# Kernel optimization log

Hardware: AMD Instinct MI355X
Metric: run time of the kernel (lower is better)

Reference implementation:

```python
import jax, jax.numpy as jnp
import numpy as np

B, T, H, W, D, NH, DEPTH, NCODES = 2, 16, 16, 16, 512, 8, 6, 1024
HW = H * W; DH = D // NH; KH = KW = 3; SIZE = KH * KW; MLP_DIM = 2 * D
NEG = -1e9


def _ln(x, g, b, eps=1e-5):
    m = jnp.mean(x, -1, keepdims=True)
    v = jnp.mean((x - m) ** 2, -1, keepdims=True)
    return (x - m) * jax.lax.rsqrt(v + eps) * g + b


def _rope(x, pos):
    # x: [N, h, T, dh]; half-split rotary embedding
    half = x.shape[-1] // 2
    freqs = 1.0 / (10000.0 ** (jnp.arange(half, dtype=jnp.float32) / half))
    ang = pos[:, None] * freqs[None]            # [T, half]
    cos = jnp.concatenate([jnp.cos(ang), jnp.cos(ang)], -1)
    sin = jnp.concatenate([jnp.sin(ang), jnp.sin(ang)], -1)
    rot = jnp.concatenate([-x[..., half:], x[..., :half]], -1)
    return x * cos + rot * sin


def setup_inputs() -> dict:
    key = jax.random.key(0)
    keys = iter(jax.random.split(key, 64))
    def p(shape, s=0.02):
        return (s * jax.random.normal(next(keys), shape)).astype(jnp.float32)
    inp = dict(
        codes=jax.random.randint(next(keys), (B, T, HW), 0, NCODES),
        emb_table=p((NCODES, D)),
        cls_token=p((1, 1, 1, D)),
        h_emb=p((1, 1, H, D)),
        w_emb=p((1, 1, W, D)),
        emb_norm_g=jnp.ones(D), emb_norm_b=jnp.zeros(D),
        sn_g=jnp.ones((DEPTH, D)), sn_b=jnp.zeros((DEPTH, D)),
        s_wq=p((DEPTH, D, D)), s_bq=jnp.zeros((DEPTH, D)),
        s_wk=p((DEPTH, D, D)), s_bk=jnp.zeros((DEPTH, D)),
        s_wv=p((DEPTH, D, D)), s_bv=jnp.zeros((DEPTH, D)),
        s_wo=p((DEPTH, D, D)), s_bo=jnp.zeros((DEPTH, D)),
        tn_g=jnp.ones((DEPTH, D)), tn_b=jnp.zeros((DEPTH, D)),
        t_wq=p((DEPTH, D, D)), t_bq=jnp.zeros((DEPTH, D)),
        t_wk=p((DEPTH, D, D)), t_bk=jnp.zeros((DEPTH, D)),
        t_wv=p((DEPTH, D, D)), t_bv=jnp.zeros((DEPTH, D)),
        t_wo=p((DEPTH, D, D)), t_bo=jnp.zeros((DEPTH, D)),
        mn_g=jnp.ones((DEPTH, D)), mn_b=jnp.zeros((DEPTH, D)),
        mlp_w1=p((DEPTH, D, MLP_DIM)), mlp_b1=jnp.zeros((DEPTH, MLP_DIM)),
        mlp_w2=p((DEPTH, MLP_DIM, D)), mlp_b2=jnp.zeros((DEPTH, D)),
        fn_g=jnp.ones(D), fn_b=jnp.zeros(D),
    )
    return inp


def reference(codes, emb_table, cls_token, h_emb, w_emb, emb_norm_g, emb_norm_b,
              sn_g, sn_b, s_wq, s_bq, s_wk, s_bk, s_wv, s_bv, s_wo, s_bo,
              tn_g, tn_b, t_wq, t_bq, t_wk, t_bk, t_wv, t_bv, t_wo, t_bo,
              mn_g, mn_b, mlp_w1, mlp_b1, mlp_w2, mlp_b2, fn_g, fn_b):
    T1 = T + 1
    emb = emb_table[codes]                                   # [B,T,HW,D]
    # positional embeddings exactly as torch repeat / repeat_interleave
    x = emb + jnp.tile(h_emb, (1, 1, W, 1)) + jnp.repeat(w_emb, H, axis=2)
    x = jnp.concatenate([x, jnp.broadcast_to(cls_token, (B, 1, HW, D))], axis=1)
    x = _ln(x, emb_norm_g, emb_norm_b)                       # [B,T1,HW,D]

    # temporal causal mask: True = masked
    tmask = jnp.triu(jnp.ones((T1, T1), dtype=bool), 1).at[-1, -1].set(True)
    # spatial out-of-bounds mask [H,W,SIZE] from unfold of ones with zero pad
    ones_pad = jnp.pad(jnp.ones((H, W), jnp.float32), 1)
    smask = jnp.stack([ones_pad[a:a + H, b:b + W]
                       for a in range(KH) for b in range(KW)], -1) == 0

    scale = 1.0 / jnp.sqrt(jnp.float32(DH))
    pos = jnp.arange(T1, dtype=jnp.float32)
    k_list, v_list = [], []
    attn_logits = None
    for i in range(DEPTH):
        # ---- spatial windowed attention on frames 0..T-1 ----
        xg = x[:, :-1].reshape(B, T, H, W, D)
        xn = _ln(xg, sn_g[i], sn_b[i])
        pad = jnp.pad(xn, ((0, 0), (0, 0), (1, 1), (1, 1), (0, 0)))
        nb = jnp.stack([pad[:, :, a:a + H, b:b + W]
                        for a in range(KH) for b in range(KW)], axis=4)  # [B,T,H,W,SIZE,D]
        q = (xn @ s_wq[i] + s_bq[i]).reshape(B, T, H, W, NH, DH)
        kk = (nb @ s_wk[i] + s_bk[i]).reshape(B, T, H, W, SIZE, NH, DH)
        vv = (nb @ s_wv[i] + s_bv[i]).reshape(B, T, H, W, SIZE, NH, DH)
        lg = jnp.einsum('btxynd,btxysnd->btxyns', q, kk) * scale
        lg = jnp.where(smask[None, None, :, :, None, :], NEG, lg)
        a_sp = jax.nn.softmax(lg, -1)
        o = jnp.einsum('btxyns,btxysnd->btxynd', a_sp, vv).reshape(B, T, H, W, D)
        o = o @ s_wo[i] + s_bo[i]
        x_sp = (o + xg).reshape(B, T, HW, D)                 # residual (drop_path=id, eval)
        xt = jnp.concatenate([x_sp, x[:, -1:]], axis=1)      # [B,T1,HW,D]

        # ---- temporal RoPE causal attention over T1 per spatial location ----
        s = xt.transpose(0, 2, 1, 3).reshape(B * HW, T1, D)
        sn_ = _ln(s, tn_g[i], tn_b[i])
        def heads(y):
            return y.reshape(B * HW, T1, NH, DH).transpose(0, 2, 1, 3)
        qt = _rope(heads(sn_ @ t_wq[i] + t_bq[i]), pos)
        kt = _rope(heads(sn_ @ t_wk[i] + t_bk[i]), pos)
        vt = heads(sn_ @ t_wv[i] + t_bv[i])
        lt = jnp.einsum('nhqd,nhkd->nhqk', qt, kt) * scale
        lt = jnp.where(tmask[None, None], NEG, lt)
        at = jax.nn.softmax(lt, -1)
        ot = jnp.einsum('nhqk,nhkd->nhqd', at, vt).transpose(0, 2, 1, 3).reshape(B * HW, T1, D)
        s = (ot @ t_wo[i] + t_bo[i]) + s
        xo = s.reshape(B, HW, T1, D).transpose(0, 2, 1, 3)   # [B,T1,HW,D]
        # average frame 0 over HW and broadcast back (as in torch code)
        xo = xo.at[:, 0].set(jnp.broadcast_to(xo[:, 0].mean(axis=1, keepdims=True), (B, HW, D)))
        attn_logits = lt.reshape(B, HW, NH, T1, T1)

        # ---- MLP (dim -> 2*dim, tanh, -> dim), dropout off in eval ----
        y = jnp.tanh(_ln(xo, mn_g[i], mn_b[i]) @ mlp_w1[i] + mlp_b1[i]) @ mlp_w2[i] + mlp_b2[i]
        x = y + xo
        k_list.append(kt[:, :, :-1, :])
        v_list.append(vt[:, :, :-1, :])

    return _ln(x, fn_g, fn_b), attn_logits, jnp.stack(k_list), jnp.stack(v_list)
```

## Files before the change

kernel.cpp:

```cpp
#include <hip/hip_runtime.h>
#include <hip/hip_bf16.h>
#include <math.h>

#define D_    512
#define NHH   8
#define DH_   64
#define T_    16
#define T1_   17
#define HWL   256
#define B__   2
#define NEGV  -1e9f

typedef __attribute__((ext_vector_type(8))) short short8;
typedef __attribute__((ext_vector_type(4))) short short4v;
typedef __attribute__((ext_vector_type(4))) float f32x4;
typedef __hip_bfloat16 bf16;

__device__ inline float wave_sum(float v){
  #pragma unroll
  for(int o=32;o>0;o>>=1) v += __shfl_xor(v,o,64);
  return v;
}
__device__ inline float b2f(unsigned short s){
  unsigned u = ((unsigned)s)<<16; float f; __builtin_memcpy(&f,&u,4); return f;
}
__device__ inline short f2bs(float f){
  bf16 h = __float2bfloat16(f); short s; __builtin_memcpy(&s,&h,2); return s;
}
__device__ inline void gload_lds16(const void* g, void* l){
  __builtin_amdgcn_global_load_lds((const __attribute__((address_space(1))) void*)g,
                                   (__attribute__((address_space(3))) void*)l, 16, 0, 0);
}

__global__ __launch_bounds__(256) void embed_ln_kernel(
    const int* __restrict__ codes, const float* __restrict__ emb,
    const float* __restrict__ cls, const float* __restrict__ hpos,
    const float* __restrict__ wpos, const float* __restrict__ g,
    const float* __restrict__ bta, float* __restrict__ X){
  int row  = blockIdx.x*4 + (threadIdx.x>>6);
  int lane = threadIdx.x & 63;
  int hw = row % HWL; int bt = row / HWL; int t = bt % T1_; int bb = bt / T1_;
  float v[8];
  if(t < T_){
    int code = codes[(bb*T_ + t)*HWL + hw];
    const float* ep = emb  + (size_t)code*D_;
    const float* hp = hpos + (size_t)(hw & 15)*D_;
    const float* wp = wpos + (size_t)(hw >> 4)*D_;
    #pragma unroll
    for(int j=0;j<8;j++){ int d = lane + j*64; v[j] = ep[d] + hp[d] + wp[d]; }
  } else {
    #pragma unroll
    for(int j=0;j<8;j++) v[j] = cls[lane + j*64];
  }
  float s=0;
  #pragma unroll
  for(int j=0;j<8;j++) s += v[j];
  s = wave_sum(s);
  float mean = s*(1.f/512.f);
  float s2=0;
  #pragma unroll
  for(int j=0;j<8;j++){ float d0=v[j]-mean; s2 += d0*d0; }
  s2 = wave_sum(s2);
  float inv = rsqrtf(s2*(1.f/512.f) + 1e-5f);
  float* o = X + (size_t)row*D_;
  #pragma unroll
  for(int j=0;j<8;j++){ int d = lane + j*64; o[d] = (v[j]-mean)*inv*g[d] + bta[d]; }
}

__global__ __launch_bounds__(256) void ln_kernel(
    const float* __restrict__ in, float* __restrict__ out,
    const float* __restrict__ g, const float* __restrict__ bta,
    int c_rpb, int s_rpb){
  int row  = blockIdx.x*4 + (threadIdx.x>>6);
  int lane = threadIdx.x & 63;
  int bb = row / c_rpb; int rem = row - bb*c_rpb;
  const float4* p = (const float4*)(in + ((size_t)bb*s_rpb + rem)*D_);
  float4 a = p[lane], c = p[lane+64];
  float s = a.x+a.y+a.z+a.w + c.x+c.y+c.z+c.w;
  s = wave_sum(s);
  float mean = s*(1.f/512.f);
  float s2 = (a.x-mean)*(a.x-mean)+(a.y-mean)*(a.y-mean)+(a.z-mean)*(a.z-mean)+(a.w-mean)*(a.w-mean)
           + (c.x-mean)*(c.x-mean)+(c.y-mean)*(c.y-mean)+(c.z-mean)*(c.z-mean)+(c.w-mean)*(c.w-mean);
  s2 = wave_sum(s2);
  float inv = rsqrtf(s2*(1.f/512.f) + 1e-5f);
  const float4* g4 = (const float4*)g; const float4* b4 = (const float4*)bta;
  float4 gv=g4[lane], gw=g4[lane+64], bv=b4[lane], bw=b4[lane+64];
  float4 o0 = { (a.x-mean)*inv*gv.x+bv.x, (a.y-mean)*inv*gv.y+bv.y,
                (a.z-mean)*inv*gv.z+bv.z, (a.w-mean)*inv*gv.w+bv.w };
  float4 o1 = { (c.x-mean)*inv*gw.x+bw.x, (c.y-mean)*inv*gw.y+bw.y,
                (c.z-mean)*inv*gw.z+bw.z, (c.w-mean)*inv*gw.w+bw.w };
  float4* o = (float4*)(out + (size_t)row*D_);
  o[lane] = o0; o[lane+64] = o1;
}

__global__ __launch_bounds__(256) void ln_bf_kernel(
    const float* __restrict__ in, bf16* __restrict__ out,
    const float* __restrict__ g, const float* __restrict__ bta,
    int c_rpb, int s_rpb){
  int row  = blockIdx.x*4 + (threadIdx.x>>6);
  int lane = threadIdx.x & 63;
  int bb = row / c_rpb; int rem = row - bb*c_rpb;
  const float4* p = (const float4*)(in + ((size_t)bb*s_rpb + rem)*D_);
  float4 a = p[lane], c = p[lane+64];
  float s = a.x+a.y+a.z+a.w + c.x+c.y+c.z+c.w;
  s = wave_sum(s);
  float mean = s*(1.f/512.f);
  float s2 = (a.x-mean)*(a.x-mean)+(a.y-mean)*(a.y-mean)+(a.z-mean)*(a.z-mean)+(a.w-mean)*(a.w-mean)
           + (c.x-mean)*(c.x-mean)+(c.y-mean)*(c.y-mean)+(c.z-mean)*(c.z-mean)+(c.w-mean)*(c.w-mean);
  s2 = wave_sum(s2);
  float inv = rsqrtf(s2*(1.f/512.f) + 1e-5f);
  const float4* g4 = (const float4*)g; const float4* b4 = (const float4*)bta;
  float4 gv=g4[lane], gw=g4[lane+64], bv=b4[lane], bw=b4[lane+64];
  short4v r0 = { f2bs((a.x-mean)*inv*gv.x+bv.x), f2bs((a.y-mean)*inv*gv.y+bv.y),
                 f2bs((a.z-mean)*inv*gv.z+bv.z), f2bs((a.w-mean)*inv*gv.w+bv.w) };
  short4v r1 = { f2bs((c.x-mean)*inv*gw.x+bw.x), f2bs((c.y-mean)*inv*gw.y+bw.y),
                 f2bs((c.z-mean)*inv*gw.z+bw.z), f2bs((c.w-mean)*inv*gw.w+bw.w) };
  bf16* o = out + (size_t)row*D_;
  *(short4v*)&o[lane*4]       = r0;
  *(short4v*)&o[256 + lane*4] = r1;
}

__global__ __launch_bounds__(256) void wconv_kernel(
    const float* sq, const float* sk, const float* sv, const float* so,
    const float* tq, const float* tk, const float* tv, const float* to,
    const float* w1, const float* w2, bf16* __restrict__ dst){
  __shared__ float sm[32][33];
  int z = blockIdx.z; int i = z/10, id = z - i*10;
  const size_t wo = (size_t)i*262144, mo = (size_t)i*524288;
  bf16* db = dst + (size_t)i*3145728;
  const float* src; bf16* d; int K, N;
  switch(id){
    case 0: src=sq+wo; d=db+0*262144;  K=512;  N=512;  break;
    case 1: src=sk+wo; d=db+1*262144;  K=512;  N=512;  break;
    case 2: src=sv+wo; d=db+2*262144;  K=512;  N=512;  break;
    case 3: src=so+wo; d=db+3*262144;  K=512;  N=512;  break;
    case 4: src=tq+wo; d=db+4*262144;  K=512;  N=512;  break;
    case 5: src=tk+wo; d=db+5*262144;  K=512;  N=512;  break;
    case 6: src=tv+wo; d=db+6*262144;  K=512;  N=512;  break;
    case 7: src=to+wo; d=db+7*262144;  K=512;  N=512;  break;
    case 8: src=w1+mo; d=db+2097152;   K=512;  N=1024; break;
    default:src=w2+mo; d=db+2621440;   K=1024; N=512;  break;
  }
  int n0 = blockIdx.x<<5, k0 = blockIdx.y<<5;
  if(n0 >= N || k0 >= K) return;
  int tx = threadIdx.x & 31, ty = threadIdx.x >> 5;
  #pragma unroll
  for(int j=0;j<4;j++) sm[ty+j*8][tx] = src[(size_t)(k0+ty+j*8)*N + n0+tx];
  __syncthreads();
  #pragma unroll
  for(int j=0;j<4;j++) d[(size_t)(n0+ty+j*8)*K + k0+tx] = __float2bfloat16(sm[tx][ty+j*8]);
}

template<int ACT, bool RES, bool OBF>
__global__ __launch_bounds__(256) void gemm_mfma(
    const bf16* __restrict__ A, const bf16* __restrict__ Wt,
    const float* __restrict__ bias, void* __restrict__ outp,
    const float* __restrict__ resid, int K, int N, int c_rpb, int o_rpb){
  __shared__ __align__(16) bf16 As[128*64];
  __shared__ __align__(16) bf16 Bs[128*64];
  const int tid  = threadIdx.x;
  const int lane = tid & 63;
  const int w    = tid >> 6;
  const int row0 = blockIdx.y << 7;
  const int col0 = blockIdx.x << 7;
  const int mb = (w>>1)*64, nb = (w&1)*64;
  size_t ga[4], gb[4];
  #pragma unroll
  for(int r=0;r<4;r++){
    int c = (r*4+w)*64 + lane;
    int rw = c>>3;
    int ks = (c&7) ^ (rw&7);
    ga[r] = (size_t)(row0+rw)*K + (ks<<3);
    gb[r] = (size_t)(col0+rw)*K + (ks<<3);
  }
  f32x4 acc[4][4] = {};
  for(int k0=0;k0<K;k0+=64){
    #pragma unroll
    for(int r=0;r<4;r++){
      gload_lds16(A  + ga[r] + k0, As + (size_t)(r*4+w)*512);
      gload_lds16(Wt + gb[r] + k0, Bs + (size_t)(r*4+w)*512);
    }
    __syncthreads();
    const short8* Av = (const short8*)As;
    const short8* Bv = (const short8*)Bs;
    #pragma unroll
    for(int kk=0;kk<2;kk++){
      const int slot = (lane>>4) + kk*4;
      short8 af[4], bfr[4];
      #pragma unroll
      for(int mi=0;mi<4;mi++){ int rw = mb + mi*16 + (lane&15); af[mi]  = Av[rw*8 + (slot ^ (rw&7))]; }
      #pragma unroll
      for(int ni=0;ni<4;ni++){ int rw = nb + ni*16 + (lane&15); bfr[ni] = Bv[rw*8 + (slot ^ (rw&7))]; }
      #pragma unroll
      for(int mi=0;mi<4;mi++)
        #pragma unroll
        for(int ni=0;ni<4;ni++)
          acc[mi][ni] = __builtin_amdgcn_mfma_f32_16x16x32_bf16(af[mi], bfr[ni], acc[mi][ni], 0,0,0);
    }
    __syncthreads();
  }
  #pragma unroll
  for(int mi=0;mi<4;mi++){
    #pragma unroll
    for(int r=0;r<4;r++){
      int row = row0 + mb + mi*16 + (lane>>4)*4 + r;
      int bb = row / c_rpb;
      size_t orow = (size_t)bb*o_rpb + (row - bb*c_rpb);
      #pragma unroll
      for(int ni=0;ni<4;ni++){
        int col = col0 + nb + ni*16 + (lane&15);
        float v = acc[mi][ni][r] + bias[col];
        if(ACT==1) v = tanhf(v);
        if(RES) v += resid[orow*(size_t)N + col];
        if(OBF) ((bf16*)outp)[orow*(size_t)N + col] = __float2bfloat16(v);
        else    ((float*)outp)[orow*(size_t)N + col] = v;
      }
    }
  }
}

template<int ACT, bool RES, bool OBF>
__global__ __launch_bounds__(256) void gemm_mfma64(
    const bf16* __restrict__ A, const bf16* __restrict__ Wt,
    const float* __restrict__ bias, void* __restrict__ outp,
    const float* __restrict__ resid, int K, int N, int c_rpb, int o_rpb){
  __shared__ __align__(16) bf16 As[64*64];
  __shared__ __align__(16) bf16 Bs[64*64];
  const int tid  = threadIdx.x;
  const int lane = tid & 63;
  const int w    = tid >> 6;
  const int row0 = blockIdx.y << 6;
  const int col0 = blockIdx.x << 6;
  const int mw = (w>>1)*32, nw = (w&1)*32;
  size_t ga[2], gb[2];
  #pragma unroll
  for(int r=0;r<2;r++){
    int c = (r*4+w)*64 + lane;
    int rw = c>>3;
    int ks = (c&7) ^ (rw&7);
    ga[r] = (size_t)(row0+rw)*K + (ks<<3);
    gb[r] = (size_t)(col0+rw)*K + (ks<<3);
  }
  f32x4 acc[2][2] = {};
  for(int k0=0;k0<K;k0+=64){
    #pragma unroll
    for(int r=0;r<2;r++){
      gload_lds16(A  + ga[r] + k0, As + (size_t)(r*4+w)*512);
      gload_lds16(Wt + gb[r] + k0, Bs + (size_t)(r*4+w)*512);
    }
    __syncthreads();
    const short8* Av = (const short8*)As;
    const short8* Bv = (const short8*)Bs;
    #pragma unroll
    for(int kk=0;kk<2;kk++){
      const int slot = (lane>>4) + kk*4;
      short8 af[2], bfr[2];
      #pragma unroll
      for(int mi=0;mi<2;mi++){ int rw = mw + mi*16 + (lane&15); af[mi]  = Av[rw*8 + (slot ^ (rw&7))]; }
      #pragma unroll
      for(int ni=0;ni<2;ni++){ int rw = nw + ni*16 + (lane&15); bfr[ni] = Bv[rw*8 + (slot ^ (rw&7))]; }
      #pragma unroll
      for(int mi=0;mi<2;mi++)
        #pragma unroll
        for(int ni=0;ni<2;ni++)
          acc[mi][ni] = __builtin_amdgcn_mfma_f32_16x16x32_bf16(af[mi], bfr[ni], acc[mi][ni], 0,0,0);
    }
    __syncthreads();
  }
  #pragma unroll
  for(int mi=0;mi<2;mi++){
    #pragma unroll
    for(int r=0;r<4;r++){
      int row = row0 + mw + mi*16 + (lane>>4)*4 + r;
      int bb = row / c_rpb;
      size_t orow = (size_t)bb*o_rpb + (row - bb*c_rpb);
      #pragma unroll
      for(int ni=0;ni<2;ni++){
        int col = col0 + nw + ni*16 + (lane&15);
        float v = acc[mi][ni][r] + bias[col];
        if(ACT==1) v = tanhf(v);
        if(RES) v += resid[orow*(size_t)N + col];
        if(OBF) ((bf16*)outp)[orow*(size_t)N + col] = __float2bfloat16(v);
        else    ((float*)outp)[orow*(size_t)N + col] = v;
      }
    }
  }
}

__global__ __launch_bounds__(256) void gemm_qkv(
    const bf16* __restrict__ A, const bf16* __restrict__ Wt,
    const float* __restrict__ bq, const float* __restrict__ bk, const float* __restrict__ bv,
    bf16* __restrict__ Qo, bf16* __restrict__ Ko, bf16* __restrict__ Vo){
  const int K = 512;
  __shared__ __align__(16) bf16 As[128*64];
  __shared__ __align__(16) bf16 Bs[128*64];
  const int tid  = threadIdx.x;
  const int lane = tid & 63;
  const int w    = tid >> 6;
  const int row0 = blockIdx.y << 7;
  const int col0 = blockIdx.x << 7;
  const int mb = (w>>1)*64, nb = (w&1)*64;
  size_t ga[4], gb[4];
  #pragma unroll
  for(int r=0;r<4;r++){
    int c = (r*4+w)*64 + lane;
    int rw = c>>3;
    int ks = (c&7) ^ (rw&7);
    ga[r] = (size_t)(row0+rw)*K + (ks<<3);
    gb[r] = (size_t)(col0+rw)*K + (ks<<3);
  }
  f32x4 acc[4][4] = {};
  for(int k0=0;k0<K;k0+=64){
    #pragma unroll
    for(int r=0;r<4;r++){
      gload_lds16(A  + ga[r] + k0, As + (size_t)(r*4+w)*512);
      gload_lds16(Wt + gb[r] + k0, Bs + (size_t)(r*4+w)*512);
    }
    __syncthreads();
    const short8* Av = (const short8*)As;
    const short8* Bv = (const short8*)Bs;
    #pragma unroll
    for(int kk=0;kk<2;kk++){
      const int slot = (lane>>4) + kk*4;
      short8 af[4], bfr[4];
      #pragma unroll
      for(int mi=0;mi<4;mi++){ int rw = mb + mi*16 + (lane&15); af[mi]  = Av[rw*8 + (slot ^ (rw&7))]; }
      #pragma unroll
      for(int ni=0;ni<4;ni++){ int rw = nb + ni*16 + (lane&15); bfr[ni] = Bv[rw*8 + (slot ^ (rw&7))]; }
      #pragma unroll
      for(int mi=0;mi<4;mi++)
        #pragma unroll
        for(int ni=0;ni<4;ni++)
          acc[mi][ni] = __builtin_amdgcn_mfma_f32_16x16x32_bf16(af[mi], bfr[ni], acc[mi][ni], 0,0,0);
    }
    __syncthreads();
  }
  const int sel = col0 >> 9;
  bf16* outp = (sel==0) ? Qo : (sel==1 ? Ko : Vo);
  const float* bp = (sel==0) ? bq : (sel==1 ? bk : bv);
  const int cb = col0 & 511;
  #pragma unroll
  for(int mi=0;mi<4;mi++){
    #pragma unroll
    for(int r=0;r<4;r++){
      int row = row0 + mb + mi*16 + (lane>>4)*4 + r;
      #pragma unroll
      for(int ni=0;ni<4;ni++){
        int col = cb + nb + ni*16 + (lane&15);
        outp[(size_t)row*512 + col] = __float2bfloat16(acc[mi][ni][r] + bp[col]);
      }
    }
  }
}

__global__ __launch_bounds__(256) void spatial_attn_kernel(
    const bf16* __restrict__ Q, const bf16* __restrict__ K,
    const bf16* __restrict__ V, bf16* __restrict__ O){
  int loc = blockIdx.x;
  int hw = loc & 255;
  int hh = hw >> 4, ww = hw & 15;
  int tid = threadIdx.x, lane = tid & 63, w = tid >> 6;
  int h = w*2 + (lane>>5);
  int j = lane & 31;
  size_t base = (size_t)loc*D_ + h*DH_ + 2*j;
  unsigned uq = *(const unsigned*)&Q[base];
  float q0 = b2f((unsigned short)uq), q1 = b2f((unsigned short)(uq>>16));
  float lg[9]; int nrow[9];
  #pragma unroll
  for(int s=0;s<9;s++){
    int a = s/3 - 1, b2_ = s%3 - 1;
    int nh = hh + a, nw = ww + b2_;
    bool ok = ((unsigned)nh < 16u) && ((unsigned)nw < 16u);
    nrow[s] = ok ? (loc - hw + (nh<<4) + nw) : -1;
    float p = 0.f;
    if(ok){
      unsigned uk = *(const unsigned*)&K[(size_t)nrow[s]*D_ + h*DH_ + 2*j];
      p = q0*b2f((unsigned short)uk) + q1*b2f((unsigned short)(uk>>16));
    }
    #pragma unroll
    for(int o=16;o>0;o>>=1) p += __shfl_xor(p, o, 64);
    lg[s] = ok ? p*0.125f : NEGV;
  }
  float m = lg[0];
  #pragma unroll
  for(int s=1;s<9;s++) m = fmaxf(m, lg[s]);
  float den = 0.f, wv[9];
  #pragma unroll
  for(int s=0;s<9;s++){ wv[s] = __expf(lg[s]-m); den += wv[s]; }
  float inv = 1.f/den;
  float a0 = 0.f, a1 = 0.f;
  #pragma unroll
  for(int s=0;s<9;s++){
    if(nrow[s] >= 0){
      unsigned uv = *(const unsigned*)&V[(size_t)nrow[s]*D_ + h*DH_ + 2*j];
      a0 += wv[s]*b2f((unsigned short)uv);
      a1 += wv[s]*b2f((unsigned short)(uv>>16));
    }
  }
  unsigned up = (unsigned)(unsigned short)f2bs(a0*inv) | ((unsigned)(unsigned short)f2bs(a1*inv) << 16);
  *(unsigned*)&O[base] = up;
}

__global__ __launch_bounds__(512) void fused_tattn(
    const bf16* __restrict__ Qb, const bf16* __restrict__ Kb, const bf16* __restrict__ Vb,
    bf16* __restrict__ O, float* __restrict__ kout, float* __restrict__ vout,
    float* __restrict__ ltout, int write_lt){
  __shared__ __align__(16) bf16 Qs[17*520];
  __shared__ __align__(16) bf16 Ks[17*520];
  __shared__ __align__(16) bf16 Vs[17*512];
  __shared__ float Ws[8][17][18];
  const int tid = threadIdx.x, w = tid>>6, lane = tid&63;
  const int hw = blockIdx.x & 255, b = blockIdx.x >> 8;
  const size_t tstr = (size_t)HWL*D_;
  const size_t rb0 = ((size_t)(b*T1_)*HWL + hw)*D_;
  for(int t=w; t<17; t+=8){
    size_t src = rb0 + (size_t)t*tstr + lane*8;
    *(short8*)&Qs[t*520 + lane*8] = *(const short8*)&Qb[src];
    *(short8*)&Ks[t*520 + lane*8] = *(const short8*)&Kb[src];
    *(short8*)&Vs[t*512 + lane*8] = *(const short8*)&Vb[src];
  }
  __syncthreads();
  {
    int i = lane & 31;
    float freq = __expf(-9.210340372f * (float)i * (1.f/32.f));
    bf16* P = (lane < 32) ? Qs : Ks;
    #pragma unroll
    for(int t=0;t<17;t++){
      float sn, cs; __sincosf((float)t*freq, &sn, &cs);
      int idx = t*520 + w*64 + i;
      float x1 = __bfloat162float(P[idx]);
      float x2 = __bfloat162float(P[idx+32]);
      P[idx]    = __float2bfloat16(x1*cs - x2*sn);
      P[idx+32] = __float2bfloat16(x2*cs + x1*sn);
    }
  }
  __syncthreads();
  {
    size_t eb = (((size_t)(b*HWL + hw)*NHH + w)*16)*64 + lane;
    #pragma unroll
    for(int t=0;t<16;t++){
      kout[eb + t*64] = __bfloat162float(Ks[t*520 + w*64 + lane]);
      vout[eb + t*64] = __bfloat162float(Vs[t*512 + w*64 + lane]);
    }
  }
  size_t lb = ((size_t)(b*HWL + hw)*NHH + w)*289;
  for(int p=lane; p<289; p+=64){
    int t = p/17, u = p - t*17;
    float d = 0.f;
    #pragma unroll
    for(int jj=0;jj<8;jj++){
      short8 qq = *(short8*)&Qs[t*520 + w*64 + jj*8];
      short8 kk = *(short8*)&Ks[u*520 + w*64 + jj*8];
      #pragma unroll
      for(int e=0;e<8;e++) d += b2f((unsigned short)qq[e]) * b2f((unsigned short)kk[e]);
    }
    bool masked = (u > t) || (t == 16 && u == 16);
    float lg = masked ? NEGV : d*0.125f;
    Ws[w][t][u] = lg;
    if(write_lt) ltout[lb + t*17 + u] = lg;
  }
  __syncthreads();
  if(lane < 17){
    float m = -1e30f;
    #pragma unroll
    for(int u=0;u<17;u++) m = fmaxf(m, Ws[w][lane][u]);
    float den = 0.f, e[17];
    #pragma unroll
    for(int u=0;u<17;u++){ e[u] = __expf(Ws[w][lane][u]-m); den += e[u]; }
    float inv = 1.f/den;
    #pragma unroll
    for(int u=0;u<17;u++) Ws[w][lane][u] = e[u]*inv;
  }
  __syncthreads();
  float Vr[17];
  #pragma unroll
  for(int u=0;u<17;u++) Vr[u] = __bfloat162float(Vs[u*512 + w*64 + lane]);
  #pragma unroll
  for(int t=0;t<17;t++){
    float acc = 0.f;
    #pragma unroll
    for(int u=0;u<17;u++) acc += Ws[w][t][u]*Vr[u];
    O[rb0 + (size_t)t*tstr + w*64 + lane] = __float2bfloat16(acc);
  }
}

__global__ __launch_bounds__(256) void avg_frame0_kernel(float* __restrict__ X){
  int d = blockIdx.x & 511; int bb = blockIdx.x >> 9;
  int hw = threadIdx.x;
  __shared__ float sm[256];
  size_t idx = ((size_t)(bb*T1_)*HWL + hw)*D_ + d;
  sm[hw] = X[idx];
  __syncthreads();
  for(int o=128;o>0;o>>=1){ if(hw<o) sm[hw] += sm[hw+o]; __syncthreads(); }
  X[idx] = sm[0]*(1.f/256.f);
}

extern "C" void kernel_launch(void* const* d_in, const int* in_sizes, int n_in,
                              void* d_out, int out_size, void* d_ws, size_t ws_size,
                              hipStream_t stream){
  const int*   codes = (const int*)  d_in[0];
  const float* emb   = (const float*)d_in[1];
  const float* cls   = (const float*)d_in[2];
  const float* hpos  = (const float*)d_in[3];
  const float* wpos  = (const float*)d_in[4];
  const float* eng   = (const float*)d_in[5];
  const float* enb   = (const float*)d_in[6];
  const float* sn_g  = (const float*)d_in[7];
  const float* sn_b  = (const float*)d_in[8];
  const float* s_wq  = (const float*)d_in[9];
  const float* s_bq  = (const float*)d_in[10];
  const float* s_wk  = (const float*)d_in[11];
  const float* s_bk  = (const float*)d_in[12];
  const float* s_wv  = (const float*)d_in[13];
  const float* s_bv  = (const float*)d_in[14];
  const float* s_wo  = (const float*)d_in[15];
  const float* s_bo  = (const float*)d_in[16];
  const float* tn_g  = (const float*)d_in[17];
  const float* tn_b  = (const float*)d_in[18];
  const float* t_wq  = (const float*)d_in[19];
  const float* t_bq  = (const float*)d_in[20];
  const float* t_wk  = (const float*)d_in[21];
  const float* t_bk  = (const float*)d_in[22];
  const float* t_wv  = (const float*)d_in[23];
  const float* t_bv  = (const float*)d_in[24];
  const float* t_wo  = (const float*)d_in[25];
  const float* t_bo  = (const float*)d_in[26];
  const float* mn_g  = (const float*)d_in[27];
  const float* mn_b  = (const float*)d_in[28];
  const float* mw1   = (const float*)d_in[29];
  const float* mb1   = (const float*)d_in[30];
  const float* mw2   = (const float*)d_in[31];
  const float* mb2   = (const float*)d_in[32];
  const float* fn_g  = (const float*)d_in[33];
  const float* fn_b  = (const float*)d_in[34];

  float* ws = (float*)d_ws;
  const size_t NX = 4456448;
  float* X   = ws;
  bf16*  XNb = (bf16*)(X + NX);
  bf16*  Qb  = (bf16*)((float*)XNb + NX/2);
  bf16*  Kb  = (bf16*)((float*)Qb  + NX/2);
  bf16*  Vb  = (bf16*)((float*)Kb  + NX/2);
  bf16*  Wt  = (bf16*)((float*)Vb  + NX/2);
  bf16*  HIDb= Qb;

  float* out0 = (float*)d_out;
  float* out1 = out0 + NX;
  float* out2 = out1 + 1183744;
  float* out3 = out2 + 25165824;

  const int RS = B__*T_*HWL;
  const int RT = B__*T1_*HWL;
  dim3 gQs(12, 64);
  dim3 gQt(12, 68);
  dim3 g64s(8, 128);
  dim3 g64t(8, 136);
  dim3 gM1(8, 68);
  dim3 wcg(32, 32, 60);

  embed_ln_kernel<<<RT/4, 256, 0, stream>>>(codes, emb, cls, hpos, wpos, eng, enb, X);
  wconv_kernel<<<wcg,256,0,stream>>>(s_wq, s_wk, s_wv, s_wo, t_wq, t_wk, t_wv, t_wo, mw1, mw2, Wt);

  for(int i=0;i<6;i++){
    bf16* Wl = Wt + (size_t)i*3145728;
    ln_bf_kernel<<<RS/4,256,0,stream>>>(X, XNb, sn_g+i*D_, sn_b+i*D_, T_*HWL, T1_*HWL);
    gemm_qkv<<<gQs,256,0,stream>>>(XNb, Wl, s_bq+i*D_, s_bk+i*D_, s_bv+i*D_, Qb, Kb, Vb);
    spatial_attn_kernel<<<RS,256,0,stream>>>(Qb, Kb, Vb, XNb);
    gemm_mfma64<0,true,false><<<g64s,256,0,stream>>>(XNb, Wl+3*262144, s_bo+i*D_, X, X, 512, 512, T_*HWL, T1_*HWL);
    ln_bf_kernel<<<RT/4,256,0,stream>>>(X, XNb, tn_g+i*D_, tn_b+i*D_, T1_*HWL, T1_*HWL);
    gemm_qkv<<<gQt,256,0,stream>>>(XNb, Wl+4*262144, t_bq+i*D_, t_bk+i*D_, t_bv+i*D_, Qb, Kb, Vb);
    fused_tattn<<<512,512,0,stream>>>(Qb, Kb, Vb, XNb,
                                      out2+(size_t)i*4194304, out3+(size_t)i*4194304,
                                      out1, (i==5)?1:0);
    gemm_mfma64<0,true,false><<<g64t,256,0,stream>>>(XNb, Wl+7*262144, t_bo+i*D_, X, X, 512, 512, RT, RT);
    avg_frame0_kernel<<<1024,256,0,stream>>>(X);
    ln_bf_kernel<<<RT/4,256,0,stream>>>(X, XNb, mn_g+i*D_, mn_b+i*D_, T1_*HWL, T1_*HWL);
    gemm_mfma<1,false,true ><<<gM1,256,0,stream>>>(XNb, Wl+2097152, mb1+i*1024, HIDb, nullptr, 512, 1024, RT, RT);
    gemm_mfma64<0,true,false><<<g64t,256,0,stream>>>(HIDb, Wl+2621440, mb2+i*D_, X, X, 1024, 512, RT, RT);
  }
  ln_kernel<<<RT/4,256,0,stream>>>(X, out0, fn_g, fn_b, T1_*HWL, T1_*HWL);
}
```

Measured before the change: 1.362 ms.

## Store residual stream in bf16 and double-buffer the 64-tile GEMM

Switches the residual activation buffer X from fp32 to bf16 across embedding, all layer norms, residual GEMM epilogues, frame-0 averaging and the final norm. The aim is to halve the memory traffic spent reading and writing the residual stream. It also adds LDS double buffering to gemm_mfma64, so the next K-tile loads while the current one is computed, and vectorises the embedding loads. The cost is accumulated rounding error in the residual over six layers, which could hurt accuracy against the fp32 reference.

New measurement: 1.363 ms. No clear change (+0.1%).

```diff
diff --git a/kernel.cpp b/kernel.cpp
--- a/kernel.cpp
+++ b/kernel.cpp
@@ -36,21 +36,25 @@
     const int* __restrict__ codes, const float* __restrict__ emb,
     const float* __restrict__ cls, const float* __restrict__ hpos,
     const float* __restrict__ wpos, const float* __restrict__ g,
-    const float* __restrict__ bta, float* __restrict__ X){
+    const float* __restrict__ bta, bf16* __restrict__ X){
   int row  = blockIdx.x*4 + (threadIdx.x>>6);
   int lane = threadIdx.x & 63;
   int hw = row % HWL; int bt = row / HWL; int t = bt % T1_; int bb = bt / T1_;
   float v[8];
   if(t < T_){
     int code = codes[(bb*T_ + t)*HWL + hw];
-    const float* ep = emb  + (size_t)code*D_;
-    const float* hp = hpos + (size_t)(hw & 15)*D_;
-    const float* wp = wpos + (size_t)(hw >> 4)*D_;
-    #pragma unroll
-    for(int j=0;j<8;j++){ int d = lane + j*64; v[j] = ep[d] + hp[d] + wp[d]; }
+    const float4* ep = (const float4*)(emb  + (size_t)code*D_);
+    const float4* hp = (const float4*)(hpos + (size_t)(hw & 15)*D_);
+    const float4* wp = (const float4*)(wpos + (size_t)(hw >> 4)*D_);
+    float4 a0=ep[lane*2], a1=ep[lane*2+1];
+    float4 h0=hp[lane*2], h1=hp[lane*2+1];
+    float4 w0=wp[lane*2], w1=wp[lane*2+1];
+    v[0]=a0.x+h0.x+w0.x; v[1]=a0.y+h0.y+w0.y; v[2]=a0.z+h0.z+w0.z; v[3]=a0.w+h0.w+w0.w;
+    v[4]=a1.x+h1.x+w1.x; v[5]=a1.y+h1.y+w1.y; v[6]=a1.z+h1.z+w1.z; v[7]=a1.w+h1.w+w1.w;
   } else {
-    #pragma unroll
-    for(int j=0;j<8;j++) v[j] = cls[lane + j*64];
+    const float4* cp = (const float4*)cls;
+    float4 c0=cp[lane*2], c1=cp[lane*2+1];
+    v[0]=c0.x; v[1]=c0.y; v[2]=c0.z; v[3]=c0.w; v[4]=c1.x; v[5]=c1.y; v[6]=c1.z; v[7]=c1.w;
   }
   float s=0;
   #pragma unroll
@@ -62,62 +66,73 @@
   for(int j=0;j<8;j++){ float d0=v[j]-mean; s2 += d0*d0; }
   s2 = wave_sum(s2);
   float inv = rsqrtf(s2*(1.f/512.f) + 1e-5f);
-  float* o = X + (size_t)row*D_;
-  #pragma unroll
-  for(int j=0;j<8;j++){ int d = lane + j*64; o[d] = (v[j]-mean)*inv*g[d] + bta[d]; }
+  const float4* g4 = (const float4*)g; const float4* b4 = (const float4*)bta;
+  float4 gv=g4[lane*2], gw=g4[lane*2+1], bv=b4[lane*2], bw=b4[lane*2+1];
+  short4v r0 = { f2bs((v[0]-mean)*inv*gv.x+bv.x), f2bs((v[1]-mean)*inv*gv.y+bv.y),
+                 f2bs((v[2]-mean)*inv*gv.z+bv.z), f2bs((v[3]-mean)*inv*gv.w+bv.w) };
+  short4v r1 = { f2bs((v[4]-mean)*inv*gw.x+bw.x), f2bs((v[5]-mean)*inv*gw.y+bw.y),
+                 f2bs((v[6]-mean)*inv*gw.z+bw.z), f2bs((v[7]-mean)*inv*gw.w+bw.w) };
+  bf16* o = X + (size_t)row*D_;
+  *(short4v*)&o[lane*8]     = r0;
+  *(short4v*)&o[lane*8 + 4] = r1;
 }
 
 __global__ __launch_bounds__(256) void ln_kernel(
-    const float* __restrict__ in, float* __restrict__ out,
+    const bf16* __restrict__ in, float* __restrict__ out,
     const float* __restrict__ g, const float* __restrict__ bta,
     int c_rpb, int s_rpb){
   int row  = blockIdx.x*4 + (threadIdx.x>>6);
   int lane = threadIdx.x & 63;
   int bb = row / c_rpb; int rem = row - bb*c_rpb;
-  const float4* p = (const float4*)(in + ((size_t)bb*s_rpb + rem)*D_);
-  float4 a = p[lane], c = p[lane+64];
-  float s = a.x+a.y+a.z+a.w + c.x+c.y+c.z+c.w;
+  short8 vv = *(const short8*)(in + ((size_t)bb*s_rpb + rem)*D_ + lane*8);
+  float v[8]; float s=0;
+  #pragma unroll
+  for(int j=0;j<8;j++){ v[j] = b2f((unsigned short)vv[j]); s += v[j]; }
   s = wave_sum(s);
   float mean = s*(1.f/512.f);
-  float s2 = (a.x-mean)*(a.x-mean)+(a.y-mean)*(a.y-mean)+(a.z-mean)*(a.z-mean)+(a.w-mean)*(a.w-mean)
-           + (c.x-mean)*(c.x-mean)+(c.y-mean)*(c.y-mean)+(c.z-mean)*(c.z-mean)+(c.w-mean)*(c.w-mean);
+  float s2=0;
+  #pragma unroll
+  for(int j=0;j<8;j++){ float d0=v[j]-mean; s2 += d0*d0; }
   s2 = wave_sum(s2);
   float inv = rsqrtf(s2*(1.f/512.f) + 1e-5f);
   const float4* g4 = (const float4*)g; const float4* b4 = (const float4*)bta;
-  float4 gv=g4[lane], gw=g4[lane+64], bv=b4[lane], bw=b4[lane+64];
-  float4 o0 = { (a.x-mean)*inv*gv.x+bv.x, (a.y-mean)*inv*gv.y+bv.y,
-                (a.z-mean)*inv*gv.z+bv.z, (a.w-mean)*inv*gv.w+bv.w };
-  float4 o1 = { (c.x-mean)*inv*gw.x+bw.x, (c.y-mean)*inv*gw.y+bw.y,
-                (c.z-mean)*inv*gw.z+bw.z, (c.w-mean)*inv*gw.w+bw.w };
-  float4* o = (float4*)(out + (size_t)row*D_);
-  o[lane] = o0; o[lane+64] = o1;
+  float4 gv=g4[lane*2], gw=g4[lane*2+1], bv=b4[lane*2], bw=b4[lane*2+1];
+  float4 o0 = { (v[0]-mean)*inv*gv.x+bv.x, (v[1]-mean)*inv*gv.y+bv.y,
+                (v[2]-mean)*inv*gv.z+bv.z, (v[3]-mean)*inv*gv.w+bv.w };
+  float4 o1 = { (v[4]-mean)*inv*gw.x+bw.x, (v[5]-mean)*inv*gw.y+bw.y,
+                (v[6]-mean)*inv*gw.z+bw.z, (v[7]-mean)*inv*gw.w+bw.w };
+  float* o = out + (size_t)row*D_;
+  *(float4*)&o[lane*8]     = o0;
+  *(float4*)&o[lane*8 + 4] = o1;
 }
 
 __global__ __launch_bounds__(256) void ln_bf_kernel(
-    const float* __restrict__ in, bf16* __restrict__ out,
+    const bf16* __restrict__ in, bf16* __restrict__ out,
     const float* __restrict__ g, const float* __restrict__ bta,
     int c_rpb, int s_rpb){
   int row  = blockIdx.x*4 + (threadIdx.x>>6);
   int lane = threadIdx.x & 63;
   int bb = row / c_rpb; int rem = row - bb*c_rpb;
-  const float4* p = (const float4*)(in + ((size_t)bb*s_rpb + rem)*D_);
-  float4 a = p[lane], c = p[lane+64];
-  float s = a.x+a.y+a.z+a.w + c.x+c.y+c.z+c.w;
+  short8 vv = *(const short8*)(in + ((size_t)bb*s_rpb + rem)*D_ + lane*8);
+  float v[8]; float s=0;
+  #pragma unroll
+  for(int j=0;j<8;j++){ v[j] = b2f((unsigned short)vv[j]); s += v[j]; }
   s = wave_sum(s);
   float mean = s*(1.f/512.f);
-  float s2 = (a.x-mean)*(a.x-mean)+(a.y-mean)*(a.y-mean)+(a.z-mean)*(a.z-mean)+(a.w-mean)*(a.w-mean)
-           + (c.x-mean)*(c.x-mean)+(c.y-mean)*(c.y-mean)+(c.z-mean)*(c.z-mean)+(c.w-mean)*(c.w-mean);
+  float s2=0;
+  #pragma unroll
+  for(int j=0;j<8;j++){ float d0=v[j]-mean; s2 += d0*d0; }
   s2 = wave_sum(s2);
   float inv = rsqrtf(s2*(1.f/512.f) + 1e-5f);
   const float4* g4 = (const float4*)g; const float4* b4 = (const float4*)bta;
-  float4 gv=g4[lane], gw=g4[lane+64], bv=b4[lane], bw=b4[lane+64];
-  short4v r0 = { f2bs((a.x-mean)*inv*gv.x+bv.x), f2bs((a.y-mean)*inv*gv.y+bv.y),
-                 f2bs((a.z-mean)*inv*gv.z+bv.z), f2bs((a.w-mean)*inv*gv.w+bv.w) };
-  short4v r1 = { f2bs((c.x-mean)*inv*gw.x+bw.x), f2bs((c.y-mean)*inv*gw.y+bw.y),
-                 f2bs((c.z-mean)*inv*gw.z+bw.z), f2bs((c.w-mean)*inv*gw.w+bw.w) };
+  float4 gv=g4[lane*2], gw=g4[lane*2+1], bv=b4[lane*2], bw=b4[lane*2+1];
+  short4v r0 = { f2bs((v[0]-mean)*inv*gv.x+bv.x), f2bs((v[1]-mean)*inv*gv.y+bv.y),
+                 f2bs((v[2]-mean)*inv*gv.z+bv.z), f2bs((v[3]-mean)*inv*gv.w+bv.w) };
+  short4v r1 = { f2bs((v[4]-mean)*inv*gw.x+bw.x), f2bs((v[5]-mean)*inv*gw.y+bw.y),
+                 f2bs((v[6]-mean)*inv*gw.z+bw.z), f2bs((v[7]-mean)*inv*gw.w+bw.w) };
   bf16* o = out + (size_t)row*D_;
-  *(short4v*)&o[lane*4]       = r0;
-  *(short4v*)&o[256 + lane*4] = r1;
+  *(short4v*)&o[lane*8]     = r0;
+  *(short4v*)&o[lane*8 + 4] = r1;
 }
 
 __global__ __launch_bounds__(256) void wconv_kernel(
@@ -155,7 +170,7 @@
 __global__ __launch_bounds__(256) void gemm_mfma(
     const bf16* __restrict__ A, const bf16* __restrict__ Wt,
     const float* __restrict__ bias, void* __restrict__ outp,
-    const float* __restrict__ resid, int K, int N, int c_rpb, int o_rpb){
+    const bf16* __restrict__ resid, int K, int N, int c_rpb, int o_rpb){
   __shared__ __align__(16) bf16 As[128*64];
   __shared__ __align__(16) bf16 Bs[128*64];
   const int tid  = threadIdx.x;
@@ -211,7 +226,7 @@
         int col = col0 + nb + ni*16 + (lane&15);
         float v = acc[mi][ni][r] + bias[col];
         if(ACT==1) v = tanhf(v);
-        if(RES) v += resid[orow*(size_t)N + col];
+        if(RES) v += __bfloat162float(resid[orow*(size_t)N + col]);
         if(OBF) ((bf16*)outp)[orow*(size_t)N + col] = __float2bfloat16(v);
         else    ((float*)outp)[orow*(size_t)N + col] = v;
       }
@@ -219,13 +234,12 @@
   }
 }
 
-template<int ACT, bool RES, bool OBF>
 __global__ __launch_bounds__(256) void gemm_mfma64(
     const bf16* __restrict__ A, const bf16* __restrict__ Wt,
-    const float* __restrict__ bias, void* __restrict__ outp,
-    const float* __restrict__ resid, int K, int N, int c_rpb, int o_rpb){
-  __shared__ __align__(16) bf16 As[64*64];
-  __shared__ __align__(16) bf16 Bs[64*64];
+    const float* __restrict__ bias, bf16* __restrict__ outp,
+    const bf16* __restrict__ resid, int K, int N, int c_rpb, int o_rpb){
+  __shared__ __align__(16) bf16 As[2][64*64];
+  __shared__ __align__(16) bf16 Bs[2][64*64];
   const int tid  = threadIdx.x;
   const int lane = tid & 63;
   const int w    = tid >> 6;
@@ -242,15 +256,23 @@
     gb[r] = (size_t)(col0+rw)*K + (ks<<3);
   }
   f32x4 acc[2][2] = {};
+  #pragma unroll
+  for(int r=0;r<2;r++){
+    gload_lds16(A  + ga[r], &As[0][(r*4+w)*512]);
+    gload_lds16(Wt + gb[r], &Bs[0][(r*4+w)*512]);
+  }
+  __syncthreads();
+  int cur = 0;
   for(int k0=0;k0<K;k0+=64){
-    #pragma unroll
-    for(int r=0;r<2;r++){
-      gload_lds16(A  + ga[r] + k0, As + (size_t)(r*4+w)*512);
-      gload_lds16(Wt + gb[r] + k0, Bs + (size_t)(r*4+w)*512);
-    }
-    __syncthreads();
-    const short8* Av = (const short8*)As;
-    const short8* Bv = (const short8*)Bs;
+    if(k0+64 < K){
+      #pragma unroll
+      for(int r=0;r<2;r++){
+        gload_lds16(A  + ga[r] + k0+64, &As[cur^1][(r*4+w)*512]);
+        gload_lds16(Wt + gb[r] + k0+64, &Bs[cur^1][(r*4+w)*512]);
+      }
+    }
+    const short8* Av = (const short8*)As[cur];
+    const short8* Bv = (const short8*)Bs[cur];
     #pragma unroll
     for(int kk=0;kk<2;kk++){
       const int slot = (lane>>4) + kk*4;
@@ -266,6 +288,7 @@
           acc[mi][ni] = __builtin_amdgcn_mfma_f32_16x16x32_bf16(af[mi], bfr[ni], acc[mi][ni], 0,0,0);
     }
     __syncthreads();
+    cur ^= 1;
   }
   #pragma unroll
   for(int mi=0;mi<2;mi++){
@@ -278,10 +301,8 @@
       for(int ni=0;ni<2;ni++){
         int col = col0 + nw + ni*16 + (lane&15);
         float v = acc[mi][ni][r] + bias[col];
-        if(ACT==1) v = tanhf(v);
-        if(RES) v += resid[orow*(size_t)N + col];
-        if(OBF) ((bf16*)outp)[orow*(size_t)N + col] = __float2bfloat16(v);
-        else    ((float*)outp)[orow*(size_t)N + col] = v;
+        v += __bfloat162float(resid[orow*(size_t)N + col]);
+        outp[orow*(size_t)N + col] = __float2bfloat16(v);
       }
     }
   }
@@ -484,15 +505,15 @@
   }
 }
 
-__global__ __launch_bounds__(256) void avg_frame0_kernel(float* __restrict__ X){
+__global__ __launch_bounds__(256) void avg_frame0_kernel(bf16* __restrict__ X){
   int d = blockIdx.x & 511; int bb = blockIdx.x >> 9;
   int hw = threadIdx.x;
   __shared__ float sm[256];
   size_t idx = ((size_t)(bb*T1_)*HWL + hw)*D_ + d;
-  sm[hw] = X[idx];
+  sm[hw] = __bfloat162float(X[idx]);
   __syncthreads();
   for(int o=128;o>0;o>>=1){ if(hw<o) sm[hw] += sm[hw+o]; __syncthreads(); }
-  X[idx] = sm[0]*(1.f/256.f);
+  X[idx] = __float2bfloat16(sm[0]*(1.f/256.f));
 }
 
 extern "C" void kernel_launch(void* const* d_in, const int* in_sizes, int n_in,
@@ -534,15 +555,14 @@
   const float* fn_g  = (const float*)d_in[33];
   const float* fn_b  = (const float*)d_in[34];
 
-  float* ws = (float*)d_ws;
   const size_t NX = 4456448;
-  float* X   = ws;
-  bf16*  XNb = (bf16*)(X + NX);
-  bf16*  Qb  = (bf16*)((float*)XNb + NX/2);
-  bf16*  Kb  = (bf16*)((float*)Qb  + NX/2);
-  bf16*  Vb  = (bf16*)((float*)Kb  + NX/2);
-  bf16*  Wt  = (bf16*)((float*)Vb  + NX/2);
-  bf16*  HIDb= Qb;
+  bf16* Xb  = (bf16*)d_ws;
+  bf16* XNb = Xb  + NX;
+  bf16* Qb  = XNb + NX;
+  bf16* Kb  = Qb  + NX;
+  bf16* Vb  = Kb  + NX;
+  bf16* Wt  = Vb  + NX;
+  bf16* HIDb= Qb;
 
   float* out0 = (float*)d_out;
   float* out1 = out0 + NX;
@@ -558,25 +578,25 @@
   dim3 gM1(8, 68);
   dim3 wcg(32, 32, 60);
 
-  embed_ln_kernel<<<RT/4, 256, 0, stream>>>(codes, emb, cls, hpos, wpos, eng, enb, X);
+  embed_ln_kernel<<<RT/4, 256, 0, stream>>>(codes, emb, cls, hpos, wpos, eng, enb, Xb);
   wconv_kernel<<<wcg,256,0,stream>>>(s_wq, s_wk, s_wv, s_wo, t_wq, t_wk, t_wv, t_wo, mw1, mw2, Wt);
 
   for(int i=0;i<6;i++){
     bf16* Wl = Wt + (size_t)i*3145728;
-    ln_bf_kernel<<<RS/4,256,0,stream>>>(X, XNb, sn_g+i*D_, sn_b+i*D_, T_*HWL, T1_*HWL);
+    ln_bf_kernel<<<RS/4,256,0,stream>>>(Xb, XNb, sn_g+i*D_, sn_b+i*D_, T_*HWL, T1_*HWL);
     gemm_qkv<<<gQs,256,0,stream>>>(XNb, Wl, s_bq+i*D_, s_bk+i*D_, s_bv+i*D_, Qb, Kb, Vb);
     spatial_attn_kernel<<<RS,256,0,stream>>>(Qb, Kb, Vb, XNb);
-    gemm_mfma64<0,true,false><<<g64s,256,0,stream>>>(XNb, Wl+3*262144, s_bo+i*D_, X, X, 512, 512, T_*HWL, T1_*HWL);
-    ln_bf_kernel<<<RT/4,256,0,stream>>>(X, XNb, tn_g+i*D_, tn_b+i*D_, T1_*HWL, T1_*HWL);
+    gemm_mfma64<<<g64s,256,0,stream>>>(XNb, Wl+3*262144, s_bo+i*D_, Xb, Xb, 512, 512, T_*HWL, T1_*HWL);
+    ln_bf_kernel<<<RT/4,256,0,stream>>>(Xb, XNb, tn_g+i*D_, tn_b+i*D_, T1_*HWL, T1_*HWL);
     gemm_qkv<<<gQt,256,0,stream>>>(XNb, Wl+4*262144, t_bq+i*D_, t_bk+i*D_, t_bv+i*D_, Qb, Kb, Vb);
     fused_tattn<<<512,512,0,stream>>>(Qb, Kb, Vb, XNb,
                                       out2+(size_t)i*4194304, out3+(size_t)i*4194304,
                                       out1, (i==5)?1:0);
-    gemm_mfma64<0,true,false><<<g64t,256,0,stream>>>(XNb, Wl+7*262144, t_bo+i*D_, X, X, 512, 512, RT, RT);
-    avg_frame0_kernel<<<1024,256,0,stream>>>(X);
-    ln_bf_kernel<<<RT/4,256,0,stream>>>(X, XNb, mn_g+i*D_, mn_b+i*D_, T1_*HWL, T1_*HWL);
+    gemm_mfma64<<<g64t,256,0,stream>>>(XNb, Wl+7*262144, t_bo+i*D_, Xb, Xb, 512, 512, RT, RT);
+    avg_frame0_kernel<<<1024,256,0,stream>>>(Xb);
+    ln_bf_kernel<<<RT/4,256,0,stream>>>(Xb, XNb, mn_g+i*D_, mn_b+i*D_, T1_*HWL, T1_*HWL);
     gemm_mfma<1,false,true ><<<gM1,256,0,stream>>>(XNb, Wl+2097152, mb1+i*1024, HIDb, nullptr, 512, 1024, RT, RT);
-    gemm_mfma64<0,true,false><<<g64t,256,0,stream>>>(HIDb, Wl+2621440, mb2+i*D_, X, X, 1024, 512, RT, RT);
-  }
-  ln_kernel<<<RT/4,256,0,stream>>>(X, out0, fn_g, fn_b, T1_*HWL, T1_*HWL);
-}
+    gemm_mfma64<<<g64t,256,0,stream>>>(HIDb, Wl+2621440, mb2+i*D_, Xb, Xb, 1024, 512, RT, RT);
+  }
+  ln_kernel<<<RT/4,256,0,stream>>>(Xb, out0, fn_g, fn_b, T1_*HWL, T1_*HWL);
+}
```
